# Performance work log

Hardware: AMD Instinct MI355X
Metric: run time of the kernel (lower is better)

The kernel has to match this reference:

```python
import jax, jax.numpy as jnp
import numpy as np

B, N = 8, 128          # batch, nodes
D = 256                # message_size (== resized node/edge feature size)
LH = 512               # link_hidden_size
P = 3                  # propagate_layers
C = 117                # hoi_classes
DE, DN = 200, 100      # raw edge / node feature sizes


def setup_inputs() -> dict:
    key = jax.random.key(0)
    ks = jax.random.split(key, 12)
    g = lambda k, sh, s=0.05: jax.random.normal(k, sh, dtype=jnp.float32) * s
    return {
        "edge_features": jax.random.normal(ks[0], (B, N, N, DE), dtype=jnp.float32),
        "node_features": jax.random.normal(ks[1], (B, N, DN), dtype=jnp.float32),
        # feature resize linears
        "W_er": g(ks[2], (D, DE)), "b_er": jnp.zeros((D,), jnp.float32),
        "W_nr": g(ks[3], (D, DN)), "b_nr": jnp.zeros((D,), jnp.float32),
        # link function: GraphConv = per-edge MLP (1x1 convs), last layer -> 1 channel
        "Wl1": g(ks[4], (LH, D)), "bl1": jnp.zeros((LH,), jnp.float32),
        "Wl2": g(ks[5], (LH, LH)), "bl2": jnp.zeros((LH,), jnp.float32),
        "Wl3": g(ks[6], (1, LH)), "bl3": jnp.zeros((1,), jnp.float32),
        # message function: Linear(concat(h_w, e_vw)) + ReLU
        "W_m": g(ks[7], (D, 2 * D)), "b_m": jnp.zeros((D,), jnp.float32),
        # GRU update (single layer): torch GRU weight layout [r; z; n]
        "W_ih": g(ks[8], (3 * D, D)), "b_ih": jnp.zeros((3 * D,), jnp.float32),
        "W_hh": g(ks[9], (3 * D, D)), "b_hh": jnp.zeros((3 * D,), jnp.float32),
        # readout fc
        "W_r": g(ks[10], (C, D)), "b_r": jnp.zeros((C,), jnp.float32),
    }


def reference(edge_features, node_features, W_er, b_er, W_nr, b_nr,
              Wl1, bl1, Wl2, bl2, Wl3, bl3, W_m, b_m,
              W_ih, b_ih, W_hh, b_hh, W_r, b_r):
    # resize raw features to message size
    ef = edge_features @ W_er.T + b_er           # [B,N_i,N_w,D] (target i, source w)
    h = node_features @ W_nr.T + b_nr            # [B,N,D] node hidden states

    e_state = ef                                  # hidden edge state fed to link fun
    pred_adj = None
    for _ in range(P):
        # link function: per-edge MLP (equivalent to 1x1 Conv2d stack), 1-channel out
        x = jax.nn.relu(e_state @ Wl1.T + bl1)
        x = jax.nn.relu(x @ Wl2.T + bl2)
        pred_adj = (x @ Wl3.T + bl3)[..., 0]      # [B,N,N] pre-sigmoid adjacency
        sig = jax.nn.sigmoid(pred_adj)

        # messages m(i<-w) = relu(Linear([h_w ; e_{i,w}])), gated by sigmoid adj
        hw = jnp.broadcast_to(h[:, None, :, :], ef.shape)  # [B,N_i,N_w,D]
        M = jax.nn.relu(jnp.concatenate([hw, ef], axis=-1) @ W_m.T + b_m)
        M = sig[..., None] * M                    # [B,N_i,N_w,D]

        # torch code writes m_v into hidden_edge_states[...][:, :, :, i] -> transpose (i,w)
        e_state = jnp.transpose(M, (0, 2, 1, 3))

        # aggregate over sources, GRU single-step update (input=m, hidden=h)
        m = M.sum(axis=2)                         # [B,N,D]
        gi = m @ W_ih.T + b_ih
        gh = h @ W_hh.T + b_hh
        r = jax.nn.sigmoid(gi[..., :D] + gh[..., :D])
        z = jax.nn.sigmoid(gi[..., D:2 * D] + gh[..., D:2 * D])
        n = jnp.tanh(gi[..., 2 * D:] + r * gh[..., 2 * D:])
        h = (1.0 - z) * n + z * h

    pred_node_labels = h @ W_r.T + b_r            # [B,N,C]
    return pred_adj, pred_node_labels
```

## Files before the change

kernel.cpp:

```cpp
#include <hip/hip_runtime.h>
#include <math.h>

typedef unsigned short u16;
typedef __attribute__((ext_vector_type(8))) short short8;
typedef __attribute__((ext_vector_type(4))) short short4v;
typedef __attribute__((ext_vector_type(4))) float floatx4;

__device__ __forceinline__ float bf2f(u16 u) {
  union { unsigned int i; float f; } v; v.i = ((unsigned int)u) << 16; return v.f;
}
__device__ __forceinline__ u16 f2bf(float f) {
  union { unsigned int i; float f; } v; v.f = f;
  unsigned int i = v.i;
  unsigned int lsb = (i >> 16) & 1u;
  i += 0x7fffu + lsb;
  return (u16)(i >> 16);
}

__global__ __launch_bounds__(256, 2)
void fused_front_k(const float* __restrict__ edge, const u16* __restrict__ Wcomb,
                   const float* __restrict__ b_er, const float* __restrict__ cmb,
                   u16* __restrict__ es, u16* __restrict__ Em)
{
  __shared__ __align__(16) u16 As[64 * 232];
  const int tid  = threadIdx.x;
  const int lane = tid & 63;
  const int wv   = tid >> 6;
  const int q    = lane >> 4;
  const int cl   = lane & 15;
  const long r0  = (long)blockIdx.x * 64;

  for (int z = tid; z < 64 * 24; z += 256) {
    const int zr = z / 24;
    As[zr * 232 + 200 + (z - zr * 24)] = 0;
  }
  const float4* src = (const float4*)(edge + r0 * 200);
  for (int it = tid; it < 3200; it += 256) {
    const float4 v = src[it];
    const int row = it / 50;
    const int c4  = it - row * 50;
    u16 t[4] = { f2bf(v.x), f2bf(v.y), f2bf(v.z), f2bf(v.w) };
    *(short4v*)&As[row * 232 + c4 * 4] = *(short4v*)t;
  }
  __syncthreads();

  floatx4 acc[8][4];
#pragma unroll
  for (int wi = 0; wi < 8; ++wi)
#pragma unroll
    for (int ri = 0; ri < 4; ++ri)
      acc[wi][ri] = (floatx4){0.f, 0.f, 0.f, 0.f};

  short8 b0[8], b1[8];
#pragma unroll
  for (int wi = 0; wi < 8; ++wi)
    b0[wi] = *(const short8*)(Wcomb + (long)(wv * 128 + wi * 16 + cl) * 224 + q * 8);
#pragma unroll
  for (int ks = 0; ks < 7; ++ks) {
    short8* bc = (ks & 1) ? b1 : b0;
    short8* bn = (ks & 1) ? b0 : b1;
    if (ks < 6) {
      const int kb = (ks + 1) * 32;
#pragma unroll
      for (int wi = 0; wi < 8; ++wi)
        bn[wi] = *(const short8*)(Wcomb + (long)(wv * 128 + wi * 16 + cl) * 224 + kb + q * 8);
    }
    short8 a[4];
#pragma unroll
    for (int ri = 0; ri < 4; ++ri)
      a[ri] = *(const short8*)&As[(ri * 16 + cl) * 232 + ks * 32 + q * 8];
    __builtin_amdgcn_s_setprio(1);
#pragma unroll
    for (int wi = 0; wi < 8; ++wi)
#pragma unroll
      for (int ri = 0; ri < 4; ++ri)
        acc[wi][ri] = __builtin_amdgcn_mfma_f32_16x16x32_bf16(bc[wi], a[ri], acc[wi][ri], 0, 0, 0);
    __builtin_amdgcn_s_setprio(0);
  }

  const bool is_ef   = (wv < 2);
  const float* bias  = is_ef ? b_er : cmb;
  u16* dst           = is_ef ? es : Em;
  const int colbase  = (wv & 1) * 128;
#pragma unroll
  for (int wi = 0; wi < 8; ++wi) {
    const int c0i = colbase + wi * 16 + q * 4;
    const float4 bv = *(const float4*)&bias[c0i];
    const float bb[4] = {bv.x, bv.y, bv.z, bv.w};
#pragma unroll
    for (int ri = 0; ri < 4; ++ri) {
      const int row = ri * 16 + cl;
      u16 p[4];
#pragma unroll
      for (int r = 0; r < 4; ++r)
        p[r] = f2bf(acc[wi][ri][r] + bb[r]);
      *(short4v*)&dst[(r0 + row) * 256 + c0i] = *(short4v*)p;
    }
  }
}

__global__ __launch_bounds__(512, 2)
void linkmsg_k(const u16* __restrict__ es, const u16* __restrict__ Wl1b,
               const float* __restrict__ bl1, const u16* __restrict__ Wl2b,
               const float* __restrict__ bl2, const float* __restrict__ wl3,
               const float* __restrict__ bl3, const u16* __restrict__ Em,
               const float* __restrict__ Hm, float* __restrict__ adj,
               u16* __restrict__ esn,
               u16* __restrict__ msum_h, u16* __restrict__ msum_l,
               const int write_adj, const int write_es)
{
  __shared__ __align__(16) u16 x1b[128 * 512];
  const int tid  = threadIdx.x;
  const int lane = tid & 63;
  const int wv   = tid >> 6;
  const int q    = lane >> 4;
  const int cl   = lane & 15;
  const int nw0  = wv * 64;
  const long r0  = (long)blockIdx.x * 128;

  {
    const short8* gsrc = (const short8*)(es + r0 * 256);
#pragma unroll
    for (int i = 0; i < 8; ++i) {
      const int g   = tid + i * 512;
      const int row = g >> 5;
      const int c   = g & 31;
      const short8 v = gsrc[g];
      *(short8*)&x1b[row * 256 + ((c ^ (row & 15)) << 3)] = v;
    }
  }

  floatx4 acc[4][8];
#pragma unroll
  for (int ni = 0; ni < 4; ++ni)
#pragma unroll
    for (int mi = 0; mi < 8; ++mi)
      acc[ni][mi] = (floatx4){0.f, 0.f, 0.f, 0.f};

  short8 b0[4], b1[4];
#pragma unroll
  for (int ni = 0; ni < 4; ++ni)
    b0[ni] = *(const short8*)(Wl1b + (nw0 + ni * 16 + cl) * 256 + q * 8);
  __syncthreads();

  {
#pragma unroll
    for (int ks = 0; ks < 8; ++ks) {
      short8* bc = (ks & 1) ? b1 : b0;
      short8* bn = (ks & 1) ? b0 : b1;
      if (ks < 7) {
        const int kb = (ks + 1) * 32;
#pragma unroll
        for (int ni = 0; ni < 4; ++ni)
          bn[ni] = *(const short8*)(Wl1b + (nw0 + ni * 16 + cl) * 256 + kb + q * 8);
      }
      short8 a[8];
#pragma unroll
      for (int mi = 0; mi < 8; ++mi) {
        const int row = mi * 16 + cl;
        a[mi] = *(const short8*)&x1b[row * 256 + (((ks * 4 + q) ^ cl) << 3)];
      }
      __builtin_amdgcn_s_setprio(1);
#pragma unroll
      for (int ni = 0; ni < 4; ++ni)
#pragma unroll
        for (int mi = 0; mi < 8; ++mi)
          acc[ni][mi] = __builtin_amdgcn_mfma_f32_16x16x32_bf16(bc[ni], a[mi], acc[ni][mi], 0, 0, 0);
      __builtin_amdgcn_s_setprio(0);
    }
  }
  __syncthreads();

  {
#pragma unroll
    for (int ni = 0; ni < 4; ++ni) {
      const int ocb   = nw0 + ni * 16 + q * 4;
      const float4 bv = *(const float4*)&bl1[ocb];
      const float bb[4] = {bv.x, bv.y, bv.z, bv.w};
      const int chunk = ocb >> 3;
      const int off   = ocb & 7;
#pragma unroll
      for (int mi = 0; mi < 8; ++mi) {
        const int row = mi * 16 + cl;
        u16 p[4];
#pragma unroll
        for (int r = 0; r < 4; ++r)
          p[r] = f2bf(fmaxf(acc[ni][mi][r] + bb[r], 0.f));
        *(short4v*)&x1b[row * 512 + ((chunk ^ cl) << 3) + off] = *(short4v*)p;
      }
    }
  }
#pragma unroll
  for (int ni = 0; ni < 4; ++ni)
#pragma unroll
    for (int mi = 0; mi < 8; ++mi)
      acc[ni][mi] = (floatx4){0.f, 0.f, 0.f, 0.f};
  __syncthreads();

  {
    short8 c0[4], c1[4];
#pragma unroll
    for (int ni = 0; ni < 4; ++ni)
      c0[ni] = *(const short8*)(Wl2b + (nw0 + ni * 16 + cl) * 512 + q * 8);
#pragma unroll
    for (int ks = 0; ks < 16; ++ks) {
      short8* cc = (ks & 1) ? c1 : c0;
      short8* cn = (ks & 1) ? c0 : c1;
      if (ks < 15) {
        const int kb = (ks + 1) * 32;
#pragma unroll
        for (int ni = 0; ni < 4; ++ni)
          cn[ni] = *(const short8*)(Wl2b + (nw0 + ni * 16 + cl) * 512 + kb + q * 8);
      }
      short8 a[8];
#pragma unroll
      for (int mi = 0; mi < 8; ++mi) {
        const int row = mi * 16 + cl;
        a[mi] = *(const short8*)&x1b[row * 512 + (((ks * 4 + q) ^ cl) << 3)];
      }
      __builtin_amdgcn_s_setprio(1);
#pragma unroll
      for (int ni = 0; ni < 4; ++ni)
#pragma unroll
        for (int mi = 0; mi < 8; ++mi)
          acc[ni][mi] = __builtin_amdgcn_mfma_f32_16x16x32_bf16(cc[ni], a[mi], acc[ni][mi], 0, 0, 0);
      __builtin_amdgcn_s_setprio(0);
    }
  }

  float pv[8];
#pragma unroll
  for (int mi = 0; mi < 8; ++mi) pv[mi] = 0.f;
#pragma unroll
  for (int ni = 0; ni < 4; ++ni) {
    const int ocb   = nw0 + ni * 16 + q * 4;
    const float4 b2 = *(const float4*)&bl2[ocb];
    const float4 w3 = *(const float4*)&wl3[ocb];
    const float bb[4] = {b2.x, b2.y, b2.z, b2.w};
    const float ww[4] = {w3.x, w3.y, w3.z, w3.w};
#pragma unroll
    for (int mi = 0; mi < 8; ++mi) {
#pragma unroll
      for (int r = 0; r < 4; ++r)
        pv[mi] += fmaxf(acc[ni][mi][r] + bb[r], 0.f) * ww[r];
    }
  }
  __syncthreads();
  float* pf   = (float*)x1b;
  float* sigv = pf + 1024;
  float* red  = pf + 2048;
#pragma unroll
  for (int mi = 0; mi < 8; ++mi) {
    float p = pv[mi];
    p += __shfl_xor(p, 16, 64);
    p += __shfl_xor(p, 32, 64);
    if (q == 0) pf[wv * 128 + mi * 16 + cl] = p;
  }
  __syncthreads();
  if (tid < 128) {
    float s = bl3[0];
#pragma unroll
    for (int w = 0; w < 8; ++w) s += pf[w * 128 + tid];
    if (write_adj) adj[r0 + tid] = s;
    sigv[tid] = 1.f / (1.f + __expf(-s));
  }
  __syncthreads();

  const int b  = (int)(blockIdx.x >> 7);
  const int i  = (int)(blockIdx.x & 127);
  const int g  = tid >> 5;
  const int c8 = (tid & 31) * 8;
  float msacc[8] = {0.f, 0.f, 0.f, 0.f, 0.f, 0.f, 0.f, 0.f};
  for (int w0 = 0; w0 < 128; w0 += 16) {
    const int w = w0 + g;
    const float s = sigv[w];
    const short8 ev = *(const short8*)(Em + (r0 + w) * 256 + c8);
    const float4 h0 = *(const float4*)(Hm + ((long)(b * 128 + w)) * 256 + c8);
    const float4 h1 = *(const float4*)(Hm + ((long)(b * 128 + w)) * 256 + c8 + 4);
    const float hv[8] = {h0.x, h0.y, h0.z, h0.w, h1.x, h1.y, h1.z, h1.w};
    u16 mb[8];
#pragma unroll
    for (int j = 0; j < 8; ++j) {
      float x = fmaxf(bf2f(((const u16*)&ev)[j]) + hv[j], 0.f) * s;
      msacc[j] += x;
      mb[j] = f2bf(x);
    }
    if (write_es)
      *(short8*)(esn + (((long)(b * 128 + w)) * 128 + i) * 256 + c8) = *(short8*)mb;
  }
  {
    float4 m0 = {msacc[0], msacc[1], msacc[2], msacc[3]};
    float4 m1 = {msacc[4], msacc[5], msacc[6], msacc[7]};
    *(float4*)&red[tid * 8]     = m0;
    *(float4*)&red[tid * 8 + 4] = m1;
  }
  __syncthreads();
  if (tid < 256) {
    float s = 0.f;
#pragma unroll
    for (int gg = 0; gg < 16; ++gg) s += red[gg * 256 + tid];
    const long o = ((long)(b * 128 + i)) * 256 + tid;
    const u16 hi = f2bf(s);
    msum_h[o] = hi;
    msum_l[o] = f2bf(s - bf2f(hi));
  }
}

__device__ __forceinline__
void gemm_ps_dev(const u16* __restrict__ Ah, const u16* __restrict__ Al,
                 const u16* __restrict__ Bh, const u16* __restrict__ Bl,
                 const float* __restrict__ bias,
                 float* __restrict__ C, u16* __restrict__ Ch, u16* __restrict__ Cl,
                 int N, int K, int lda, int ldc, int bx, int by)
{
  __shared__ __align__(16) u16 Ash[128 * 40];
  __shared__ __align__(16) u16 Asl[128 * 40];
  __shared__ __align__(16) u16 Bsh[128 * 40];
  __shared__ __align__(16) u16 Bsl[128 * 40];
  const int tid  = threadIdx.x;
  const int m0   = bx * 128;
  const int n0   = by * 128;
  const int lane = tid & 63;
  const int wv   = tid >> 6;
  const int wm   = wv & 1;
  const int wn   = wv >> 1;
  const int q    = lane >> 4;
  const int cl   = lane & 15;

  floatx4 acc[4][4];
#pragma unroll
  for (int i = 0; i < 4; ++i)
#pragma unroll
    for (int j = 0; j < 4; ++j)
      acc[i][j] = (floatx4){0.f, 0.f, 0.f, 0.f};

  const int srow = tid >> 1;
  const int scol = (tid & 1) * 16;

  for (int kb = 0; kb < K; kb += 32) {
    {
      const long ar = (long)(m0 + srow) * lda + kb + scol;
      *(short8*)&Ash[srow * 40 + scol]     = *(const short8*)(Ah + ar);
      *(short8*)&Ash[srow * 40 + scol + 8] = *(const short8*)(Ah + ar + 8);
      *(short8*)&Asl[srow * 40 + scol]     = *(const short8*)(Al + ar);
      *(short8*)&Asl[srow * 40 + scol + 8] = *(const short8*)(Al + ar + 8);
    }
    {
      const int n = n0 + srow;
      u16* dh = &Bsh[srow * 40 + scol];
      u16* dl = &Bsl[srow * 40 + scol];
      if (n < N) {
        const long br = (long)n * K + kb + scol;
        ((short8*)dh)[0] = *(const short8*)(Bh + br);
        ((short8*)dh)[1] = *(const short8*)(Bh + br + 8);
        ((short8*)dl)[0] = *(const short8*)(Bl + br);
        ((short8*)dl)[1] = *(const short8*)(Bl + br + 8);
      } else {
#pragma unroll
        for (int j = 0; j < 16; ++j) { dh[j] = 0; dl[j] = 0; }
      }
    }
    __syncthreads();

    short8 ah[4], al[4], bh[4], bl[4];
#pragma unroll
    for (int mi = 0; mi < 4; ++mi) {
      ah[mi] = *(const short8*)&Ash[(wm * 64 + mi * 16 + cl) * 40 + q * 8];
      al[mi] = *(const short8*)&Asl[(wm * 64 + mi * 16 + cl) * 40 + q * 8];
    }
#pragma unroll
    for (int ni = 0; ni < 4; ++ni) {
      bh[ni] = *(const short8*)&Bsh[(wn * 64 + ni * 16 + cl) * 40 + q * 8];
      bl[ni] = *(const short8*)&Bsl[(wn * 64 + ni * 16 + cl) * 40 + q * 8];
    }
#pragma unroll
    for (int mi = 0; mi < 4; ++mi)
#pragma unroll
      for (int ni = 0; ni < 4; ++ni) {
        acc[mi][ni] = __builtin_amdgcn_mfma_f32_16x16x32_bf16(ah[mi], bh[ni], acc[mi][ni], 0, 0, 0);
        acc[mi][ni] = __builtin_amdgcn_mfma_f32_16x16x32_bf16(al[mi], bh[ni], acc[mi][ni], 0, 0, 0);
        acc[mi][ni] = __builtin_amdgcn_mfma_f32_16x16x32_bf16(ah[mi], bl[ni], acc[mi][ni], 0, 0, 0);
      }
    __syncthreads();
  }

#pragma unroll
  for (int mi = 0; mi < 4; ++mi) {
    const int row = m0 + wm * 64 + mi * 16 + q * 4;
#pragma unroll
    for (int ni = 0; ni < 4; ++ni) {
      const int col = n0 + wn * 64 + ni * 16 + cl;
      if (col < N) {
        const float b = bias ? bias[col] : 0.f;
#pragma unroll
        for (int r = 0; r < 4; ++r) {
          float v = acc[mi][ni][r] + b;
          const long o = (long)(row + r) * ldc + col;
          C[o] = v;
          if (Ch) {
            const u16 hi = f2bf(v);
            Ch[o] = hi;
            Cl[o] = f2bf(v - bf2f(hi));
          }
        }
      }
    }
  }
}

__global__ __launch_bounds__(256, 2)
void gemm_ps_k(const u16* __restrict__ Ah, const u16* __restrict__ Al,
               const u16* __restrict__ Bh, const u16* __restrict__ Bl,
               const float* __restrict__ bias,
               float* __restrict__ C, u16* __restrict__ Ch, u16* __restrict__ Cl,
               int N, int K, int lda, int ldc)
{
  gemm_ps_dev(Ah, Al, Bh, Bl, bias, C, Ch, Cl, N, K, lda, ldc,
              blockIdx.x, blockIdx.y);
}

__global__ __launch_bounds__(256, 2)
void gemm_hm_gh_k(const u16* __restrict__ h_h, const u16* __restrict__ h_l,
                  const u16* __restrict__ Wmh_h, const u16* __restrict__ Wmh_l,
                  const u16* __restrict__ Whh_h, const u16* __restrict__ Whh_l,
                  const float* __restrict__ b_hh,
                  float* __restrict__ Hm, float* __restrict__ gh)
{
  __shared__ __align__(16) u16 Ash[64 * 40];
  __shared__ __align__(16) u16 Asl[64 * 40];
  __shared__ __align__(16) u16 Bsh[64 * 40];
  __shared__ __align__(16) u16 Bsl[64 * 40];
  const int tid  = threadIdx.x;
  const int m0   = blockIdx.x * 64;
  const int y    = blockIdx.y;
  const bool isHm = (y < 4);
  const int n0   = (isHm ? y : (y - 4)) * 64;
  const u16* Bh  = isHm ? Wmh_h : Whh_h;
  const u16* Bl  = isHm ? Wmh_l : Whh_l;
  const float* bias = isHm ? nullptr : b_hh;
  float* C       = isHm ? Hm : gh;
  const int ldc  = isHm ? 256 : 768;

  const int lane = tid & 63;
  const int wv   = tid >> 6;
  const int wm   = wv & 1;
  const int wn   = wv >> 1;
  const int q    = lane >> 4;
  const int cl   = lane & 15;

  floatx4 acc[2][2];
#pragma unroll
  for (int i = 0; i < 2; ++i)
#pragma unroll
    for (int j = 0; j < 2; ++j)
      acc[i][j] = (floatx4){0.f, 0.f, 0.f, 0.f};

  const int srow = tid >> 2;
  const int scol = (tid & 3) * 8;

  for (int kb = 0; kb < 256; kb += 32) {
    {
      const long ar = (long)(m0 + srow) * 256 + kb + scol;
      *(short8*)&Ash[srow * 40 + scol] = *(const short8*)(h_h + ar);
      *(short8*)&Asl[srow * 40 + scol] = *(const short8*)(h_l + ar);
      const long br = (long)(n0 + srow) * 256 + kb + scol;
      *(short8*)&Bsh[srow * 40 + scol] = *(const short8*)(Bh + br);
      *(short8*)&Bsl[srow * 40 + scol] = *(const short8*)(Bl + br);
    }
    __syncthreads();

    short8 ah[2], al[2], bh[2], bl[2];
#pragma unroll
    for (int mi = 0; mi < 2; ++mi) {
      ah[mi] = *(const short8*)&Ash[(wm * 32 + mi * 16 + cl) * 40 + q * 8];
      al[mi] = *(const short8*)&Asl[(wm * 32 + mi * 16 + cl) * 40 + q * 8];
    }
#pragma unroll
    for (int ni = 0; ni < 2; ++ni) {
      bh[ni] = *(const short8*)&Bsh[(wn * 32 + ni * 16 + cl) * 40 + q * 8];
      bl[ni] = *(const short8*)&Bsl[(wn * 32 + ni * 16 + cl) * 40 + q * 8];
    }
#pragma unroll
    for (int mi = 0; mi < 2; ++mi)
#pragma unroll
      for (int ni = 0; ni < 2; ++ni) {
        acc[mi][ni] = __builtin_amdgcn_mfma_f32_16x16x32_bf16(ah[mi], bh[ni], acc[mi][ni], 0, 0, 0);
        acc[mi][ni] = __builtin_amdgcn_mfma_f32_16x16x32_bf16(al[mi], bh[ni], acc[mi][ni], 0, 0, 0);
        acc[mi][ni] = __builtin_amdgcn_mfma_f32_16x16x32_bf16(ah[mi], bl[ni], acc[mi][ni], 0, 0, 0);
      }
    __syncthreads();
  }

#pragma unroll
  for (int mi = 0; mi < 2; ++mi) {
    const int row = m0 + wm * 32 + mi * 16 + q * 4;
#pragma unroll
    for (int ni = 0; ni < 2; ++ni) {
      const int col = n0 + wn * 32 + ni * 16 + cl;
      const float b = bias ? bias[col] : 0.f;
#pragma unroll
      for (int r = 0; r < 4; ++r)
        C[(long)(row + r) * ldc + col] = acc[mi][ni][r] + b;
    }
  }
}

__global__ __launch_bounds__(256, 2)
void gemm_gru_k(const u16* __restrict__ Ah, const u16* __restrict__ Al,
                const u16* __restrict__ Bh, const u16* __restrict__ Bl,
                const float* __restrict__ b_ih,
                const float* __restrict__ gh,
                float* __restrict__ h,
                u16* __restrict__ h_h, u16* __restrict__ h_l)
{
  __shared__ __align__(16) u16 Ash[64 * 40];
  __shared__ __align__(16) u16 Asl[64 * 40];
  __shared__ __align__(16) u16 Bsh[96 * 40];
  __shared__ __align__(16) u16 Bsl[96 * 40];
  const int tid  = threadIdx.x;
  const int m0   = blockIdx.x * 64;
  const int cb   = blockIdx.y * 32;
  const int lane = tid & 63;
  const int wv   = tid >> 6;
  const int q    = lane >> 4;
  const int cl   = lane & 15;

  floatx4 acc[3][2];
#pragma unroll
  for (int g = 0; g < 3; ++g)
#pragma unroll
    for (int ni = 0; ni < 2; ++ni)
      acc[g][ni] = (floatx4){0.f, 0.f, 0.f, 0.f};

  const int srow = tid >> 2;
  const int scol = (tid & 3) * 8;

  for (int kb = 0; kb < 256; kb += 32) {
    {
      const long ar = (long)(m0 + srow) * 256 + kb + scol;
      *(short8*)&Ash[srow * 40 + scol] = *(const short8*)(Ah + ar);
      *(short8*)&Asl[srow * 40 + scol] = *(const short8*)(Al + ar);
    }
    for (int s = tid; s < 384; s += 256) {
      const int br = s >> 2;
      const int bc = (s & 3) * 8;
      const long wrow = (long)((br >> 5) * 256 + cb + (br & 31));
      *(short8*)&Bsh[br * 40 + bc] = *(const short8*)(Bh + wrow * 256 + kb + bc);
      *(short8*)&Bsl[br * 40 + bc] = *(const short8*)(Bl + wrow * 256 + kb + bc);
    }
    __syncthreads();

    const short8 ah = *(const short8*)&Ash[(wv * 16 + cl) * 40 + q * 8];
    const short8 al = *(const short8*)&Asl[(wv * 16 + cl) * 40 + q * 8];
#pragma unroll
    for (int g = 0; g < 3; ++g)
#pragma unroll
      for (int ni = 0; ni < 2; ++ni) {
        const short8 bh = *(const short8*)&Bsh[(g * 32 + ni * 16 + cl) * 40 + q * 8];
        const short8 bl = *(const short8*)&Bsl[(g * 32 + ni * 16 + cl) * 40 + q * 8];
        acc[g][ni] = __builtin_amdgcn_mfma_f32_16x16x32_bf16(ah, bh, acc[g][ni], 0, 0, 0);
        acc[g][ni] = __builtin_amdgcn_mfma_f32_16x16x32_bf16(al, bh, acc[g][ni], 0, 0, 0);
        acc[g][ni] = __builtin_amdgcn_mfma_f32_16x16x32_bf16(ah, bl, acc[g][ni], 0, 0, 0);
      }
    __syncthreads();
  }

#pragma unroll
  for (int ni = 0; ni < 2; ++ni) {
    const int col = cb + ni * 16 + cl;
    const float bi_r = b_ih[col];
    const float bi_z = b_ih[256 + col];
    const float bi_n = b_ih[512 + col];
#pragma unroll
    for (int r = 0; r < 4; ++r) {
      const int row = m0 + wv * 16 + q * 4 + r;
      const long gb = (long)row * 768;
      const float gr = (acc[0][ni][r] + bi_r) + gh[gb + col];
      const float gz = (acc[1][ni][r] + bi_z) + gh[gb + 256 + col];
      const float rv = 1.f / (1.f + __expf(-gr));
      const float zv = 1.f / (1.f + __expf(-gz));
      const float nv = tanhf((acc[2][ni][r] + bi_n) + rv * gh[gb + 512 + col]);
      const int hidx = row * 256 + col;
      const float hv = (1.f - zv) * nv + zv * h[hidx];
      h[hidx] = hv;
      const u16 hh = f2bf(hv);
      h_h[hidx] = hh;
      h_l[hidx] = f2bf(hv - bf2f(hh));
    }
  }
}

__device__ __forceinline__
void cast_pad_dev(u16* __restrict__ dst, const float* __restrict__ src,
                  int rows, int sc, int dc, int stride, int idx)
{
  if (idx >= rows * dc) return;
  int r = idx / dc, c = idx - r * dc;
  float v = (c < sc) ? src[r * stride + c] : 0.f;
  dst[idx] = f2bf(v);
}

__device__ __forceinline__
void cast_split_dev(u16* __restrict__ dh, u16* __restrict__ dl,
                    const float* __restrict__ src,
                    int rows, int sc, int dc, int stride, int idx)
{
  if (idx >= rows * dc) return;
  int r = idx / dc, c = idx - r * dc;
  float v = (c < sc) ? src[r * stride + c] : 0.f;
  u16 hi = f2bf(v);
  dh[idx] = hi;
  dl[idx] = f2bf(v - bf2f(hi));
}

__global__ __launch_bounds__(256)
void prep_all_k(const float* __restrict__ W_er, const float* __restrict__ Wl1,
                const float* __restrict__ Wl2, const float* __restrict__ W_nr,
                const float* __restrict__ W_m, const float* __restrict__ W_ih,
                const float* __restrict__ W_hh, const float* __restrict__ W_r,
                const float* __restrict__ b_er, const float* __restrict__ b_m,
                const float* __restrict__ node,
                u16* __restrict__ Wcomb, u16* __restrict__ Wl1b,
                u16* __restrict__ Wl2b,
                u16* __restrict__ Wnr_h, u16* __restrict__ Wnr_l,
                u16* __restrict__ Wmh_h, u16* __restrict__ Wmh_l,
                u16* __restrict__ Wih_h, u16* __restrict__ Wih_l,
                u16* __restrict__ Whh_h, u16* __restrict__ Whh_l,
                u16* __restrict__ Wr_h, u16* __restrict__ Wr_l,
                u16* __restrict__ node_h, u16* __restrict__ node_l,
                float* __restrict__ cmb)
{
  const int j = blockIdx.y;
  if (j == 8) {
    if (blockIdx.x >= 256) return;
    const int o = blockIdx.x;
    const int t = threadIdx.x;
    __shared__ float wme[256];
    wme[t] = W_m[o * 512 + 256 + t];
    __syncthreads();
    if (t < 224) {
      float s = 0.f;
      if (t < 200) {
        for (int c = 0; c < 256; ++c) s += wme[c] * W_er[c * 200 + t];
      }
      Wcomb[(256 + o) * 224 + t] = f2bf(s);
    }
    if (t == 0) {
      float s = 0.f;
      for (int c = 0; c < 256; ++c) s += wme[c] * b_er[c];
      cmb[o] = s + b_m[o];
    }
    return;
  }
  const int idx = blockIdx.x * 256 + threadIdx.x;
  switch (j) {
    case 0: cast_pad_dev(Wcomb, W_er, 256, 200, 224, 200, idx); break;
    case 1: cast_pad_dev(Wl1b, Wl1, 512, 256, 256, 256, idx); break;
    case 2: cast_pad_dev(Wl2b, Wl2, 512, 512, 512, 512, idx); break;
    case 3: cast_split_dev(Wnr_h, Wnr_l, W_nr, 256, 100, 128, 100, idx); break;
    case 4: cast_split_dev(Wmh_h, Wmh_l, W_m, 256, 256, 256, 512, idx); break;
    case 5: cast_split_dev(Wih_h, Wih_l, W_ih, 768, 256, 256, 256, idx); break;
    case 6: cast_split_dev(Whh_h, Whh_l, W_hh, 768, 256, 256, 256, idx); break;
    case 7: cast_split_dev(Wr_h, Wr_l, W_r, 117, 256, 256, 256, idx); break;
    case 9: cast_split_dev(node_h, node_l, node, 1024, 100, 128, 100, idx); break;
  }
}

extern "C" void kernel_launch(void* const* d_in, const int* in_sizes, int n_in,
                              void* d_out, int out_size, void* d_ws, size_t ws_size,
                              hipStream_t stream)
{
  const float* edge = (const float*)d_in[0];
  const float* node = (const float*)d_in[1];
  const float* W_er = (const float*)d_in[2];
  const float* b_er = (const float*)d_in[3];
  const float* W_nr = (const float*)d_in[4];
  const float* b_nr = (const float*)d_in[5];
  const float* Wl1  = (const float*)d_in[6];
  const float* bl1  = (const float*)d_in[7];
  const float* Wl2  = (const float*)d_in[8];
  const float* bl2  = (const float*)d_in[9];
  const float* Wl3  = (const float*)d_in[10];
  const float* bl3  = (const float*)d_in[11];
  const float* W_m  = (const float*)d_in[12];
  const float* b_m  = (const float*)d_in[13];
  const float* W_ih = (const float*)d_in[14];
  const float* b_ih = (const float*)d_in[15];
  const float* W_hh = (const float*)d_in[16];
  const float* b_hh = (const float*)d_in[17];
  const float* W_r  = (const float*)d_in[18];
  const float* b_r  = (const float*)d_in[19];
  (void)in_sizes; (void)n_in; (void)out_size; (void)ws_size;

  float* out_adj = (float*)d_out;
  float* out_lab = (float*)d_out + 131072;

  char* ws = (char*)d_ws;
  size_t off = 0;
  auto alloc = [&](size_t bytes) -> void* {
    void* p = ws + off; off += (bytes + 255) & ~(size_t)255; return p;
  };
  const long E = 131072;
  u16*   es0  = (u16*)  alloc(E * 256 * 2);
  u16*   es1  = (u16*)  alloc(E * 256 * 2);
  u16*   Em   = (u16*)  alloc(E * 256 * 2);
  float* Hm   = (float*)alloc(1024 * 256 * 4);
  float* hbuf = (float*)alloc(1024 * 256 * 4);
  float* gh   = (float*)alloc(1024 * 768 * 4);
  u16*   h_h  = (u16*)  alloc(1024 * 256 * 2);
  u16*   h_l  = (u16*)  alloc(1024 * 256 * 2);
  u16*   ms_h = (u16*)  alloc(1024 * 256 * 2);
  u16*   ms_l = (u16*)  alloc(1024 * 256 * 2);
  u16*   node_h = (u16*)alloc(1024 * 128 * 2);
  u16*   node_l = (u16*)alloc(1024 * 128 * 2);
  u16*   Wcomb = (u16*) alloc(512 * 224 * 2);
  u16*   Wl1b = (u16*)  alloc(512 * 256 * 2);
  u16*   Wl2b = (u16*)  alloc(512 * 512 * 2);
  float* cmb  = (float*)alloc(256 * 4);
  u16* Wnr_h = (u16*)alloc(256 * 128 * 2); u16* Wnr_l = (u16*)alloc(256 * 128 * 2);
  u16* Wmh_h = (u16*)alloc(256 * 256 * 2); u16* Wmh_l = (u16*)alloc(256 * 256 * 2);
  u16* Wih_h = (u16*)alloc(768 * 256 * 2); u16* Wih_l = (u16*)alloc(768 * 256 * 2);
  u16* Whh_h = (u16*)alloc(768 * 256 * 2); u16* Whh_l = (u16*)alloc(768 * 256 * 2);
  u16* Wr_h  = (u16*)alloc(117 * 256 * 2); u16* Wr_l  = (u16*)alloc(117 * 256 * 2);

  prep_all_k<<<dim3(1024, 10), 256, 0, stream>>>(
      W_er, Wl1, Wl2, W_nr, W_m, W_ih, W_hh, W_r, b_er, b_m, node,
      Wcomb, Wl1b, Wl2b, Wnr_h, Wnr_l, Wmh_h, Wmh_l,
      Wih_h, Wih_l, Whh_h, Whh_l, Wr_h, Wr_l, node_h, node_l, cmb);

  fused_front_k<<<2048, dim3(256), 0, stream>>>(edge, Wcomb, b_er, cmb, es0, Em);
  gemm_ps_k<<<dim3(8, 2), dim3(256), 0, stream>>>(
      node_h, node_l, Wnr_h, Wnr_l, b_nr, hbuf, h_h, h_l, 256, 128, 128, 256);

  u16* esbuf[2] = { es0, es1 };
  for (int p = 0; p < 3; ++p) {
    gemm_hm_gh_k<<<dim3(16, 16), dim3(256), 0, stream>>>(
        h_h, h_l, Wmh_h, Wmh_l, Whh_h, Whh_l, b_hh, Hm, gh);
    linkmsg_k<<<1024, dim3(512), 0, stream>>>(
        esbuf[p & 1], Wl1b, bl1, Wl2b, bl2, Wl3, bl3,
        Em, Hm, out_adj, esbuf[(p + 1) & 1], ms_h, ms_l,
        (p == 2) ? 1 : 0, (p < 2) ? 1 : 0);
    gemm_gru_k<<<dim3(16, 8), dim3(256), 0, stream>>>(
        ms_h, ms_l, Wih_h, Wih_l, b_ih, gh, hbuf, h_h, h_l);
  }
  gemm_ps_k<<<dim3(8, 1), dim3(256), 0, stream>>>(
      h_h, h_l, Wr_h, Wr_l, b_r, out_lab, nullptr, nullptr, 117, 256, 256, 117);
}
```

Baseline: 777.6 us.

## Fuse GRU input GEMM and update into the link-message kernel epilogue

Drops the separate gemm_gru kernel. Each linkmsg block now keeps its summed message row in shared memory, multiplies it by a transposed fp32 W_ih with plain FMAs, then applies the GRU update and writes h, h_h and h_l directly. This removes one launch per propagation step and the msum hi/lo round trip through global memory. In exchange every block streams the full 768 KB fp32 W_ih from cache and does a serial 256-long dot product on only 384 threads, which lengthens the tail of each block.

```diff
diff --git a/kernel.cpp b/kernel.cpp
--- a/kernel.cpp
+++ b/kernel.cpp
@@ -106,7 +106,11 @@
                const float* __restrict__ bl3, const u16* __restrict__ Em,
                const float* __restrict__ Hm, float* __restrict__ adj,
                u16* __restrict__ esn,
-               u16* __restrict__ msum_h, u16* __restrict__ msum_l,
+               const float* __restrict__ WihT,
+               const float* __restrict__ b_ih,
+               const float* __restrict__ gh,
+               float* __restrict__ h,
+               u16* __restrict__ h_h, u16* __restrict__ h_l,
                const int write_adj, const int write_es)
 {
   __shared__ __align__(16) u16 x1b[128 * 512];
@@ -249,6 +253,8 @@
   float* pf   = (float*)x1b;
   float* sigv = pf + 1024;
   float* red  = pf + 2048;
+  float* msv  = pf + 6144;
+  float* giL  = pf + 6464;
 #pragma unroll
   for (int mi = 0; mi < 8; ++mi) {
     float p = pv[mi];
@@ -299,10 +305,38 @@
     float s = 0.f;
 #pragma unroll
     for (int gg = 0; gg < 16; ++gg) s += red[gg * 256 + tid];
-    const long o = ((long)(b * 128 + i)) * 256 + tid;
-    const u16 hi = f2bf(s);
-    msum_h[o] = hi;
-    msum_l[o] = f2bf(s - bf2f(hi));
+    msv[tid] = s;
+  }
+  __syncthreads();
+
+  if (tid < 384) {
+    const int o2 = tid * 2;
+    float ax = 0.f, ay = 0.f;
+#pragma unroll 4
+    for (int k = 0; k < 256; ++k) {
+      const float m = msv[k];
+      const float2 w2 = *(const float2*)&WihT[k * 768 + o2];
+      ax += m * w2.x;
+      ay += m * w2.y;
+    }
+    giL[o2]     = ax;
+    giL[o2 + 1] = ay;
+  }
+  __syncthreads();
+  if (tid < 256) {
+    const int row = (int)blockIdx.x;
+    const long gb = (long)row * 768;
+    const float gr = (giL[tid]       + b_ih[tid])       + gh[gb + tid];
+    const float gz = (giL[256 + tid] + b_ih[256 + tid]) + gh[gb + 256 + tid];
+    const float rv = 1.f / (1.f + __expf(-gr));
+    const float zv = 1.f / (1.f + __expf(-gz));
+    const float nv = tanhf((giL[512 + tid] + b_ih[512 + tid]) + rv * gh[gb + 512 + tid]);
+    const int hidx = row * 256 + tid;
+    const float hv = (1.f - zv) * nv + zv * h[hidx];
+    h[hidx] = hv;
+    const u16 hh = f2bf(hv);
+    h_h[hidx] = hh;
+    h_l[hidx] = f2bf(hv - bf2f(hh));
   }
 }
 
@@ -505,91 +539,6 @@
   }
 }
 
-__global__ __launch_bounds__(256, 2)
-void gemm_gru_k(const u16* __restrict__ Ah, const u16* __restrict__ Al,
-                const u16* __restrict__ Bh, const u16* __restrict__ Bl,
-                const float* __restrict__ b_ih,
-                const float* __restrict__ gh,
-                float* __restrict__ h,
-                u16* __restrict__ h_h, u16* __restrict__ h_l)
-{
-  __shared__ __align__(16) u16 Ash[64 * 40];
-  __shared__ __align__(16) u16 Asl[64 * 40];
-  __shared__ __align__(16) u16 Bsh[96 * 40];
-  __shared__ __align__(16) u16 Bsl[96 * 40];
-  const int tid  = threadIdx.x;
-  const int m0   = blockIdx.x * 64;
-  const int cb   = blockIdx.y * 32;
-  const int lane = tid & 63;
-  const int wv   = tid >> 6;
-  const int q    = lane >> 4;
-  const int cl   = lane & 15;
-
-  floatx4 acc[3][2];
-#pragma unroll
-  for (int g = 0; g < 3; ++g)
-#pragma unroll
-    for (int ni = 0; ni < 2; ++ni)
-      acc[g][ni] = (floatx4){0.f, 0.f, 0.f, 0.f};
-
-  const int srow = tid >> 2;
-  const int scol = (tid & 3) * 8;
-
-  for (int kb = 0; kb < 256; kb += 32) {
-    {
-      const long ar = (long)(m0 + srow) * 256 + kb + scol;
-      *(short8*)&Ash[srow * 40 + scol] = *(const short8*)(Ah + ar);
-      *(short8*)&Asl[srow * 40 + scol] = *(const short8*)(Al + ar);
-    }
-    for (int s = tid; s < 384; s += 256) {
-      const int br = s >> 2;
-      const int bc = (s & 3) * 8;
-      const long wrow = (long)((br >> 5) * 256 + cb + (br & 31));
-      *(short8*)&Bsh[br * 40 + bc] = *(const short8*)(Bh + wrow * 256 + kb + bc);
-      *(short8*)&Bsl[br * 40 + bc] = *(const short8*)(Bl + wrow * 256 + kb + bc);
-    }
-    __syncthreads();
-
-    const short8 ah = *(const short8*)&Ash[(wv * 16 + cl) * 40 + q * 8];
-    const short8 al = *(const short8*)&Asl[(wv * 16 + cl) * 40 + q * 8];
-#pragma unroll
-    for (int g = 0; g < 3; ++g)
-#pragma unroll
-      for (int ni = 0; ni < 2; ++ni) {
-        const short8 bh = *(const short8*)&Bsh[(g * 32 + ni * 16 + cl) * 40 + q * 8];
-        const short8 bl = *(const short8*)&Bsl[(g * 32 + ni * 16 + cl) * 40 + q * 8];
-        acc[g][ni] = __builtin_amdgcn_mfma_f32_16x16x32_bf16(ah, bh, acc[g][ni], 0, 0, 0);
-        acc[g][ni] = __builtin_amdgcn_mfma_f32_16x16x32_bf16(al, bh, acc[g][ni], 0, 0, 0);
-        acc[g][ni] = __builtin_amdgcn_mfma_f32_16x16x32_bf16(ah, bl, acc[g][ni], 0, 0, 0);
-      }
-    __syncthreads();
-  }
-
-#pragma unroll
-  for (int ni = 0; ni < 2; ++ni) {
-    const int col = cb + ni * 16 + cl;
-    const float bi_r = b_ih[col];
-    const float bi_z = b_ih[256 + col];
-    const float bi_n = b_ih[512 + col];
-#pragma unroll
-    for (int r = 0; r < 4; ++r) {
-      const int row = m0 + wv * 16 + q * 4 + r;
-      const long gb = (long)row * 768;
-      const float gr = (acc[0][ni][r] + bi_r) + gh[gb + col];
-      const float gz = (acc[1][ni][r] + bi_z) + gh[gb + 256 + col];
-      const float rv = 1.f / (1.f + __expf(-gr));
-      const float zv = 1.f / (1.f + __expf(-gz));
-      const float nv = tanhf((acc[2][ni][r] + bi_n) + rv * gh[gb + 512 + col]);
-      const int hidx = row * 256 + col;
-      const float hv = (1.f - zv) * nv + zv * h[hidx];
-      h[hidx] = hv;
-      const u16 hh = f2bf(hv);
-      h_h[hidx] = hh;
-      h_l[hidx] = f2bf(hv - bf2f(hh));
-    }
-  }
-}
-
 __device__ __forceinline__
 void cast_pad_dev(u16* __restrict__ dst, const float* __restrict__ src,
                   int rows, int sc, int dc, int stride, int idx)
@@ -624,7 +573,7 @@
                 u16* __restrict__ Wl2b,
                 u16* __restrict__ Wnr_h, u16* __restrict__ Wnr_l,
                 u16* __restrict__ Wmh_h, u16* __restrict__ Wmh_l,
-                u16* __restrict__ Wih_h, u16* __restrict__ Wih_l,
+                float* __restrict__ WihT,
                 u16* __restrict__ Whh_h, u16* __restrict__ Whh_l,
                 u16* __restrict__ Wr_h, u16* __restrict__ Wr_l,
                 u16* __restrict__ node_h, u16* __restrict__ node_l,
@@ -659,7 +608,13 @@
     case 2: cast_pad_dev(Wl2b, Wl2, 512, 512, 512, 512, idx); break;
     case 3: cast_split_dev(Wnr_h, Wnr_l, W_nr, 256, 100, 128, 100, idx); break;
     case 4: cast_split_dev(Wmh_h, Wmh_l, W_m, 256, 256, 256, 512, idx); break;
-    case 5: cast_split_dev(Wih_h, Wih_l, W_ih, 768, 256, 256, 256, idx); break;
+    case 5: {
+      if (idx < 196608) {
+        const int k = idx / 768;
+        const int o = idx - k * 768;
+        WihT[idx] = W_ih[o * 256 + k];
+      }
+    } break;
     case 6: cast_split_dev(Whh_h, Whh_l, W_hh, 768, 256, 256, 256, idx); break;
     case 7: cast_split_dev(Wr_h, Wr_l, W_r, 117, 256, 256, 256, idx); break;
     case 9: cast_split_dev(node_h, node_l, node, 1024, 100, 128, 100, idx); break;
@@ -709,24 +664,22 @@
   float* gh   = (float*)alloc(1024 * 768 * 4);
   u16*   h_h  = (u16*)  alloc(1024 * 256 * 2);
   u16*   h_l  = (u16*)  alloc(1024 * 256 * 2);
-  u16*   ms_h = (u16*)  alloc(1024 * 256 * 2);
-  u16*   ms_l = (u16*)  alloc(1024 * 256 * 2);
   u16*   node_h = (u16*)alloc(1024 * 128 * 2);
   u16*   node_l = (u16*)alloc(1024 * 128 * 2);
   u16*   Wcomb = (u16*) alloc(512 * 224 * 2);
   u16*   Wl1b = (u16*)  alloc(512 * 256 * 2);
   u16*   Wl2b = (u16*)  alloc(512 * 512 * 2);
+  float* WihT = (float*)alloc(256 * 768 * 4);
   float* cmb  = (float*)alloc(256 * 4);
   u16* Wnr_h = (u16*)alloc(256 * 128 * 2); u16* Wnr_l = (u16*)alloc(256 * 128 * 2);
   u16* Wmh_h = (u16*)alloc(256 * 256 * 2); u16* Wmh_l = (u16*)alloc(256 * 256 * 2);
-  u16* Wih_h = (u16*)alloc(768 * 256 * 2); u16* Wih_l = (u16*)alloc(768 * 256 * 2);
   u16* Whh_h = (u16*)alloc(768 * 256 * 2); u16* Whh_l = (u16*)alloc(768 * 256 * 2);
   u16* Wr_h  = (u16*)alloc(117 * 256 * 2); u16* Wr_l  = (u16*)alloc(117 * 256 * 2);
 
   prep_all_k<<<dim3(1024, 10), 256, 0, stream>>>(
       W_er, Wl1, Wl2, W_nr, W_m, W_ih, W_hh, W_r, b_er, b_m, node,
       Wcomb, Wl1b, Wl2b, Wnr_h, Wnr_l, Wmh_h, Wmh_l,
-      Wih_h, Wih_l, Whh_h, Whh_l, Wr_h, Wr_l, node_h, node_l, cmb);
+      WihT, Whh_h, Whh_l, Wr_h, Wr_l, node_h, node_l, cmb);
 
   fused_front_k<<<2048, dim3(256), 0, stream>>>(edge, Wcomb, b_er, cmb, es0, Em);
   gemm_ps_k<<<dim3(8, 2), dim3(256), 0, stream>>>(
@@ -738,10 +691,9 @@
         h_h, h_l, Wmh_h, Wmh_l, Whh_h, Whh_l, b_hh, Hm, gh);
     linkmsg_k<<<1024, dim3(512), 0, stream>>>(
         esbuf[p & 1], Wl1b, bl1, Wl2b, bl2, Wl3, bl3,
-        Em, Hm, out_adj, esbuf[(p + 1) & 1], ms_h, ms_l,
+        Em, Hm, out_adj, esbuf[(p + 1) & 1],
+        WihT, b_ih, gh, hbuf, h_h, h_l,
         (p == 2) ? 1 : 0, (p < 2) ? 1 : 0);
-    gemm_gru_k<<<dim3(16, 8), dim3(256), 0, stream>>>(
-        ms_h, ms_l, Wih_h, Wih_l, b_ih, gh, hbuf, h_h, h_l);
   }
   gemm_ps_k<<<dim3(8, 1), dim3(256), 0, stream>>>(
       h_h, h_l, Wr_h, Wr_l, b_r, out_lab, nullptr, nullptr, 117, 256, 256, 117);
```

Result: slower. 959.7 us (+23.4%).
